# Kernel tuning notes

Measured on AMD Instinct MI355X. Metric: run time of the kernel, lower is better.

## Reference

```python
import jax, jax.numpy as jnp
import numpy as np

K = 3
STRIDE = 1
PAD = 1


def setup_inputs() -> dict:
    key = jax.random.key(0)
    k1, k2, k3 = jax.random.split(key, 3)
    N, C, H, W = 4, 256, 64, 64
    outC = 256
    x = jax.random.normal(k1, (N, C, H, W), dtype=jnp.float32)
    # offset/mask conv params (torch inits these to 0; small random makes the test nontrivial)
    conv_offset_w = jax.random.normal(k2, (3 * K * K, C, K, K), dtype=jnp.float32) * 0.01
    conv_offset_b = jnp.zeros((3 * K * K,), dtype=jnp.float32)
    # xavier-normal scale for dcn weight
    fan = C * K * K + outC * K * K
    dcn_weight = jax.random.normal(k3, (outC, C, K, K), dtype=jnp.float32) * np.float32(np.sqrt(2.0 / fan))
    return {"x": x, "conv_offset_w": conv_offset_w, "conv_offset_b": conv_offset_b, "dcn_weight": dcn_weight}


def _dcn(x, w_off, b_off, dcn_weight):
    k, s, p = K, STRIDE, PAD
    N, C, H, W = x.shape
    outC = dcn_weight.shape[0]
    KK = k * k
    # offset/mask prediction conv
    om = jax.lax.conv_general_dilated(
        x, w_off, (s, s), [(p, p), (p, p)],
        dimension_numbers=("NCHW", "OIHW", "NCHW")) + b_off[None, :, None, None]
    offset = om[:, : 2 * KK]
    mask = jax.nn.sigmoid(om[:, 2 * KK:])
    oH = (H + 2 * p - (k - 1)) // s
    oW = (W + 2 * p - (k - 1)) // s
    # pad with an extra row/col at bottom-right so floor+1 indexing is in-bounds (as in torch code)
    px = jnp.pad(x, ((0, 0), (0, 0), (p, p + 1), (p, p + 1)))
    px = jnp.transpose(px, (0, 2, 3, 1))  # (N, H+2p+1, W+2p+1, C)
    offset = jnp.transpose(offset, (0, 2, 3, 1)).reshape(N, oH, oW, KK, 2)  # (...,(y,x))
    mask = jnp.transpose(mask, (0, 2, 3, 1))  # (N, oH, oW, KK)
    base_y = jnp.arange(oH, dtype=jnp.float32) * s + p
    base_x = jnp.arange(oW, dtype=jnp.float32) * s + p
    half = (k - 1) // 2
    inner_y = jnp.repeat(jnp.arange(k, dtype=jnp.float32) - half, k)  # kernel-tap y offsets
    inner_x = jnp.tile(jnp.arange(k, dtype=jnp.float32) - half, k)   # kernel-tap x offsets
    pos_y = base_y[None, :, None, None] + inner_y[None, None, None, :] + offset[..., 0]
    pos_x = base_x[None, None, :, None] + inner_x[None, None, None, :] + offset[..., 1]
    pos_y = jnp.clip(pos_y, 0.0, H + 2 * p - 1.0)
    pos_x = jnp.clip(pos_x, 0.0, W + 2 * p - 1.0)
    y1 = jnp.floor(pos_y)
    x1 = jnp.floor(pos_x)
    y1i = y1.astype(jnp.int32)
    x1i = x1.astype(jnp.int32)
    nidx = jnp.arange(N)[:, None, None, None]
    # bilinear gathers: each (N, oH, oW, KK, C)
    v1 = px[nidx, y1i, x1i]
    v2 = px[nidx, y1i, x1i + 1]
    v3 = px[nidx, y1i + 1, x1i]
    v4 = px[nidx, y1i + 1, x1i + 1]
    lh = (pos_y - y1)[..., None]
    lw = (pos_x - x1)[..., None]
    hh = 1.0 - lh
    hw = 1.0 - lw
    value = hh * hw * v1 + hh * lw * v2 + lh * hw * v3 + lh * lw * v4
    value = value * mask[..., None]  # modulated
    w = dcn_weight.reshape(outC, C, KK)
    # sum over in_C and kernel taps -> NCHW output
    out = jnp.einsum("nhwkc,ock->nohw", value, w)
    return out


def reference(x, conv_offset_w, conv_offset_b, dcn_weight):
    return _dcn(x, conv_offset_w, conv_offset_b, dcn_weight)
```

## Files before the change

kernel.cpp:

```cpp
#include <hip/hip_runtime.h>
#include <type_traits>


typedef __bf16 bf16x8 __attribute__((ext_vector_type(8)));
typedef float  f32x4  __attribute__((ext_vector_type(4)));
typedef unsigned short ushort8 __attribute__((ext_vector_type(8)));
typedef unsigned int   uint4v  __attribute__((ext_vector_type(4)));

#define XBF_OFF   0u
#define WREP_OFF  8388608u
#define WMAIN_OFF 8536064u
#define OM_OFF    9715712u

#define LGKM0_BAR() do { __builtin_amdgcn_s_waitcnt(0xC07F); __builtin_amdgcn_s_barrier(); } while (0)

template <int N> using ic = std::integral_constant<int, N>;

__device__ __forceinline__ unsigned short f2bf(float f) {
  unsigned int u = __float_as_uint(f);
  u += 0x7fffu + ((u >> 16) & 1u);
  return (unsigned short)(u >> 16);
}
__device__ __forceinline__ float bf2f(unsigned short h) {
  return __uint_as_float(((unsigned int)h) << 16);
}

__global__ __launch_bounds__(256) void k_pre(const float* __restrict__ x,
                                             const float* __restrict__ w_off,
                                             const float* __restrict__ dcn_w,
                                             unsigned short* __restrict__ xbf,
                                             unsigned short* __restrict__ wrep,
                                             unsigned short* __restrict__ wmain) {
  __shared__ float tile[32][65];
  __shared__ unsigned short lsh[2304];
  int b = blockIdx.x;
  int t = threadIdx.x;
  if (b < 2048) {
    int n  = b >> 9;
    int cb = (b >> 6) & 7;
    int xb = b & 63;
    int xx  = t & 63;
    int cc0 = t >> 6;
#pragma unroll
    for (int j = 0; j < 8; ++j) {
      int cc = cc0 + j * 4;
      tile[cc][xx] = x[((size_t)(n * 256 + cb * 32 + cc) << 12) + xb * 64 + xx];
    }
    __syncthreads();
    int ccw = t & 31;
    int xw0 = t >> 5;
#pragma unroll
    for (int j = 0; j < 8; ++j) {
      int xw = xw0 + j * 8;
      xbf[((size_t)((n << 12) + xb * 64 + xw)) * 256 + cb * 32 + ccw] = f2bf(tile[ccw][xw]);
    }
  } else {
    int ocb = b - 2048;
    const float* src;
    unsigned short* dst;
    int oc;
    if (ocb < 32) { oc = ocb; src = w_off; dst = wrep; }
    else          { oc = ocb - 32; src = dcn_w; dst = wmain; }
    if (ocb < 32 && oc >= 27) {
#pragma unroll
      for (int j = 0; j < 9; ++j) dst[oc * 2304 + j * 256 + t] = 0;
      return;
    }
    const float* base = src + (size_t)oc * 2304;
#pragma unroll
    for (int j = 0; j < 9; ++j) lsh[j * 256 + t] = f2bf(base[t * 9 + j]);
    __syncthreads();
#pragma unroll
    for (int j = 0; j < 9; ++j) dst[oc * 2304 + j * 256 + t] = lsh[j * 256 + t];
  }
}

__global__ __launch_bounds__(1024) void k_offconv(const unsigned short* __restrict__ xbf,
                                                  const unsigned short* __restrict__ wrep,
                                                  const float* __restrict__ bias,
                                                  float* __restrict__ om) {
  __shared__ __align__(16) unsigned short SHa[4][64 * 64];
  __shared__ __align__(16) unsigned short SHb[4][32 * 64];
  int t = threadIdx.x;
  int wave = t >> 6, lane = t & 63;
  int grp = wave >> 2, wv = wave & 3;
  int tg = t & 255;
  int bm = ((blockIdx.x & 7) << 5) + (blockIdx.x >> 3);
  int n = bm >> 6, oy = bm & 63;

  unsigned short* As = SHa[grp];
  unsigned short* Bs = SHb[grp];

  int arow = tg >> 2, acc4 = tg & 3;
  int brow = tg >> 3, bch = tg & 7;

  f32x4 acc0 = {0.f, 0.f, 0.f, 0.f};
  f32x4 acc1 = {0.f, 0.f, 0.f, 0.f};

  ushort8 av[2][2]; ushort8 bv[2];
  auto prefetch = [&](int ktg, auto slotc) {
    constexpr int slot = decltype(slotc)::value;
    int kk = ktg >> 2;
    int c0 = (ktg & 3) * 64;
    int dy = kk / 3 - 1, dx = kk % 3 - 1;
    int yy = oy + dy, xxg = arow + dx;
    bool ok = ((unsigned)yy < 64u) && ((unsigned)xxg < 64u);
    const unsigned short* p = xbf + (size_t)(((n * 64 + yy) * 64 + xxg) * 256 + c0 + acc4 * 16);
#pragma unroll
    for (int g = 0; g < 2; ++g)
      av[slot][g] = ok ? *(const ushort8*)(p + g * 8) : (ushort8){0,0,0,0,0,0,0,0};
    bv[slot] = *(const ushort8*)(wrep + (size_t)brow * 2304 + ktg * 64 + bch * 8);
  };

  int k0 = grp * 9;
  prefetch(k0, ic<0>{});
  prefetch(k0 + 1, ic<1>{});
  int mr = lane & 15, q = lane >> 4;

  auto step = [&](int kt, auto slotc) {
    constexpr int slot = decltype(slotc)::value;
    LGKM0_BAR();
#pragma unroll
    for (int g = 0; g < 2; ++g) {
      int ch = (acc4 * 2 + g) ^ (arow & 7);
      *(ushort8*)&As[arow * 64 + ch * 8] = av[slot][g];
    }
    { int ch = bch ^ (brow & 7);
      *(ushort8*)&Bs[brow * 64 + ch * 8] = bv[slot]; }
    if (kt + 2 < 9) prefetch(k0 + kt + 2, slotc);
    LGKM0_BAR();
#pragma unroll
    for (int kh = 0; kh < 2; ++kh) {
      int coff = ((q + kh * 4) ^ (mr & 7)) * 8;
      bf16x8 a  = *(const bf16x8*)&As[(wv * 16 + mr) * 64 + coff];
      bf16x8 b0 = *(const bf16x8*)&Bs[mr * 64 + coff];
      bf16x8 b1 = *(const bf16x8*)&Bs[(16 + mr) * 64 + coff];
      acc0 = __builtin_amdgcn_mfma_f32_16x16x32_bf16(a, b0, acc0, 0, 0, 0);
      acc1 = __builtin_amdgcn_mfma_f32_16x16x32_bf16(a, b1, acc1, 0, 0, 0);
    }
  };
  for (int kp = 0; kp < 4; ++kp) {
    step(2 * kp, ic<0>{});
    step(2 * kp + 1, ic<1>{});
  }
  step(8, ic<0>{});

  float* scratch = (float*)&SHa[0][0];
  __syncthreads();
  if (grp > 0) {
#pragma unroll
    for (int nt = 0; nt < 2; ++nt) {
      f32x4 a = nt ? acc1 : acc0;
#pragma unroll
      for (int rg = 0; rg < 4; ++rg)
        scratch[(grp - 1) * 2048 + (wv * 16 + q * 4 + rg) * 32 + nt * 16 + mr] = a[rg];
    }
  }
  __syncthreads();
  if (grp == 0) {
    int r0 = bm * 64;
#pragma unroll
    for (int nt = 0; nt < 2; ++nt) {
      f32x4 a = nt ? acc1 : acc0;
      int oc = nt * 16 + mr;
      float bvl = (oc < 27) ? bias[oc] : 0.f;
#pragma unroll
      for (int rg = 0; rg < 4; ++rg) {
        int pl = wv * 16 + q * 4 + rg;
        float v = a[rg] + bvl + scratch[pl * 32 + oc] +
                  scratch[2048 + pl * 32 + oc] + scratch[4096 + pl * 32 + oc];
        if (oc >= 18 && oc < 27) v = 1.f / (1.f + __expf(-v));
        om[(r0 + pl) * 32 + oc] = v;
      }
    }
  }
}

__global__ __launch_bounds__(1024) void k_gemm_fused(const unsigned short* __restrict__ xbf,
                                                     const float* __restrict__ om,
                                                     const unsigned short* __restrict__ wB,
                                                     float* __restrict__ out) {
  __shared__ __align__(16) unsigned short Ab[3][128 * 64];
  __shared__ __align__(16) unsigned short Bb[3][128 * 64];
  int t = threadIdx.x;
  int wave = t >> 6, lane = t & 63;
  int wm = wave & 3, wn = wave >> 2;
  int bmx = ((blockIdx.x & 7) << 4) + (blockIdx.x >> 3);
  int r0 = bmx * 128, o0 = blockIdx.y * 128;

  int srow = t >> 3;
  int sch  = (t & 7) * 8;
  int r = r0 + srow;
  int n = r >> 12, yx = r & 4095, oy = yx >> 6, ox = yx & 63;
  const unsigned short* xb = xbf + (size_t)n * (4096 * 256);
  const float* omr = om + (size_t)r * 32;
  const unsigned short* Bg = wB + (size_t)(o0 + srow) * 2304 + sch;
  int wch = ((t & 7) ^ (srow & 7)) * 8;

  f32x4 acc[2][2];
#pragma unroll
  for (int mt = 0; mt < 2; ++mt)
#pragma unroll
    for (int nt = 0; nt < 2; ++nt) acc[mt][nt] = (f32x4){0.f, 0.f, 0.f, 0.f};

  float pv_y, pv_x, pv_m;
  float cw1, cw2, cw3, cw4;
  int a1, a2, a3, a4;
  float wbuf[2][4];

  auto loadom = [&](int kk) {
    pv_y = omr[2 * kk]; pv_x = omr[2 * kk + 1]; pv_m = omr[18 + kk];
  };
  auto params = [&](int kk) {
    float py = (float)(oy + kk / 3) + pv_y;
    float px = (float)(ox + kk % 3) + pv_x;
    float m = pv_m;
    py = fminf(fmaxf(py, 0.f), 65.f);
    px = fminf(fmaxf(px, 0.f), 65.f);
    float fy = floorf(py), fx = floorf(px);
    float ly = py - fy, lx = px - fx;
    float hy = 1.f - ly, hx = 1.f - lx;
    int iy = (int)fy, ix = (int)fx;
    bool yv0 = (iy >= 1) && (iy <= 64);
    bool yv1 = (iy <= 63);
    bool xv0 = (ix >= 1) && (ix <= 64);
    bool xv1 = (ix <= 63);
    int y0 = min(max(iy - 1, 0), 63);
    int y1 = min(iy, 63);
    int x0 = min(max(ix - 1, 0), 63);
    int x1 = min(ix, 63);
    cw1 = (yv0 && xv0) ? hy * hx * m : 0.f;
    cw2 = (yv0 && xv1) ? hy * lx * m : 0.f;
    cw3 = (yv1 && xv0) ? ly * hx * m : 0.f;
    cw4 = (yv1 && xv1) ? ly * lx * m : 0.f;
    a1 = ((y0 << 6) + x0) * 256;
    a2 = ((y0 << 6) + x1) * 256;
    a3 = ((y1 << 6) + x0) * 256;
    a4 = ((y1 << 6) + x1) * 256;
  };

  ushort8 g1[2], g2[2], g3[2], g4[2], bv[2];
  auto issueA = [&](int ktg, auto slotc) {
    constexpr int slot = decltype(slotc)::value;
    wbuf[slot][0] = cw1; wbuf[slot][1] = cw2; wbuf[slot][2] = cw3; wbuf[slot][3] = cw4;
    int c = (ktg & 3) * 64 + sch;
    g1[slot] = *(const ushort8*)(xb + a1 + c);
    g2[slot] = *(const ushort8*)(xb + a2 + c);
    g3[slot] = *(const ushort8*)(xb + a3 + c);
    g4[slot] = *(const ushort8*)(xb + a4 + c);
  };
  auto issueB = [&](int ktg, auto slotc) {
    constexpr int slot = decltype(slotc)::value;
    bv[slot] = *(const ushort8*)(Bg + ktg * 64);
  };

  loadom(0);
  params(0);
  loadom(1);
  issueA(0, ic<0>{}); issueB(0, ic<0>{});
  issueA(1, ic<1>{}); issueB(1, ic<1>{});

  int mr = lane & 15, q = lane >> 4;

  auto step = [&](int k, auto slotc, auto bufc) {
    constexpr int slot = decltype(slotc)::value;
    constexpr int buf  = decltype(bufc)::value;
    uint4v rs;
#pragma unroll
    for (int p = 0; p < 4; ++p) {
      float va = wbuf[slot][0] * bf2f(g1[slot][2 * p])     + wbuf[slot][1] * bf2f(g2[slot][2 * p]) +
                 wbuf[slot][2] * bf2f(g3[slot][2 * p])     + wbuf[slot][3] * bf2f(g4[slot][2 * p]);
      float vb = wbuf[slot][0] * bf2f(g1[slot][2 * p + 1]) + wbuf[slot][1] * bf2f(g2[slot][2 * p + 1]) +
                 wbuf[slot][2] * bf2f(g3[slot][2 * p + 1]) + wbuf[slot][3] * bf2f(g4[slot][2 * p + 1]);
      unsigned ua = __float_as_uint(va) + 0x8000u;
      unsigned ub = __float_as_uint(vb) + 0x8000u;
      rs[p] = __builtin_amdgcn_perm(ub, ua, 0x07060302u);
    }
    *(uint4v*)&Ab[buf][srow * 64 + wch] = rs;
    *(ushort8*)&Bb[buf][srow * 64 + wch] = bv[slot];
    if (k + 2 < 36) {
      if (((k + 2) & 3) == 0) {
        int kk = (k + 2) >> 2;
        params(kk);
        loadom(kk < 8 ? kk + 1 : 8);
      }
      issueA(k + 2, slotc);
      issueB(k + 2, slotc);
    }
    LGKM0_BAR();
#pragma unroll
    for (int kh = 0; kh < 2; ++kh) {
      int coff = ((q + kh * 4) ^ (mr & 7)) * 8;
      bf16x8 af[2], bfv[2];
#pragma unroll
      for (int mt = 0; mt < 2; ++mt)
        af[mt] = *(const bf16x8*)&Ab[buf][(wm * 32 + mt * 16 + mr) * 64 + coff];
#pragma unroll
      for (int nt = 0; nt < 2; ++nt)
        bfv[nt] = *(const bf16x8*)&Bb[buf][(wn * 32 + nt * 16 + mr) * 64 + coff];
#pragma unroll
      for (int mt = 0; mt < 2; ++mt)
#pragma unroll
        for (int nt = 0; nt < 2; ++nt)
          acc[mt][nt] = __builtin_amdgcn_mfma_f32_16x16x32_bf16(af[mt], bfv[nt], acc[mt][nt], 0, 0, 0);
    }
  };

  for (int kp = 0; kp < 6; ++kp) {
    int k = kp * 6;
    step(k + 0, ic<0>{}, ic<0>{});
    step(k + 1, ic<1>{}, ic<1>{});
    step(k + 2, ic<0>{}, ic<2>{});
    step(k + 3, ic<1>{}, ic<0>{});
    step(k + 4, ic<0>{}, ic<1>{});
    step(k + 5, ic<1>{}, ic<2>{});
  }

#pragma unroll
  for (int mt = 0; mt < 2; ++mt)
#pragma unroll
    for (int nt = 0; nt < 2; ++nt) {
      int p = r0 + wm * 32 + mt * 16 + q * 4;
      int o = o0 + wn * 32 + nt * 16 + mr;
      int nn = p >> 12, pyx = p & 4095;
      *(f32x4*)(out + ((size_t)(nn * 256 + o) << 12) + pyx) = acc[mt][nt];
    }
}

extern "C" void kernel_launch(void* const* d_in, const int* in_sizes, int n_in,
                              void* d_out, int out_size, void* d_ws, size_t ws_size,
                              hipStream_t stream) {
  const float* x     = (const float*)d_in[0];
  const float* w_off = (const float*)d_in[1];
  const float* b_off = (const float*)d_in[2];
  const float* dcn_w = (const float*)d_in[3];
  float* out = (float*)d_out;
  char* ws = (char*)d_ws;
  unsigned short* xbf   = (unsigned short*)(ws + XBF_OFF);
  unsigned short* wrep  = (unsigned short*)(ws + WREP_OFF);
  unsigned short* wmain = (unsigned short*)(ws + WMAIN_OFF);
  float*          om    = (float*)(ws + OM_OFF);

  k_pre<<<2048 + 288, 256, 0, stream>>>(x, w_off, dcn_w, xbf, wrep, wmain);
  k_offconv<<<256, 1024, 0, stream>>>(xbf, wrep, b_off, om);
  k_gemm_fused<<<dim3(128, 2), 1024, 0, stream>>>(xbf, om, wmain, out);
}
```

Baseline: 126.4 us.

## Compute all output channels per block with B fragments loaded directly from pre-swizzled global weights

```diff
diff --git a/kernel.cpp b/kernel.cpp
--- a/kernel.cpp
+++ b/kernel.cpp
@@ -5,7 +5,8 @@
 typedef __bf16 bf16x8 __attribute__((ext_vector_type(8)));
 typedef float  f32x4  __attribute__((ext_vector_type(4)));
 typedef unsigned short ushort8 __attribute__((ext_vector_type(8)));
-typedef unsigned int   uint4v  __attribute__((ext_vector_type(4)));
+typedef unsigned short ushort4v __attribute__((ext_vector_type(4)));
+typedef unsigned int   uint2v  __attribute__((ext_vector_type(2)));
 
 #define XBF_OFF   0u
 #define WREP_OFF  8388608u
@@ -56,22 +57,30 @@
     }
   } else {
     int ocb = b - 2048;
-    const float* src;
-    unsigned short* dst;
-    int oc;
-    if (ocb < 32) { oc = ocb; src = w_off; dst = wrep; }
-    else          { oc = ocb - 32; src = dcn_w; dst = wmain; }
-    if (ocb < 32 && oc >= 27) {
-#pragma unroll
-      for (int j = 0; j < 9; ++j) dst[oc * 2304 + j * 256 + t] = 0;
-      return;
-    }
-    const float* base = src + (size_t)oc * 2304;
-#pragma unroll
-    for (int j = 0; j < 9; ++j) lsh[j * 256 + t] = f2bf(base[t * 9 + j]);
-    __syncthreads();
-#pragma unroll
-    for (int j = 0; j < 9; ++j) dst[oc * 2304 + j * 256 + t] = lsh[j * 256 + t];
+    if (ocb < 32) {
+      int oc = ocb;
+      if (oc >= 27) {
+#pragma unroll
+        for (int j = 0; j < 9; ++j) wrep[oc * 2304 + j * 256 + t] = 0;
+        return;
+      }
+      const float* base = w_off + (size_t)oc * 2304;
+#pragma unroll
+      for (int j = 0; j < 9; ++j) lsh[j * 256 + t] = f2bf(base[t * 9 + j]);
+      __syncthreads();
+#pragma unroll
+      for (int j = 0; j < 9; ++j) wrep[oc * 2304 + j * 256 + t] = lsh[j * 256 + t];
+    } else {
+      int oc = ocb - 32;
+      const float* base = dcn_w + (size_t)oc * 2304;
+      int oco = ((oc >> 4) << 9) + (oc & 15) * 8;
+#pragma unroll
+      for (int j = 0; j < 9; ++j) {
+        int k = j * 256 + t;
+        wmain[((k >> 5) << 13) + oco + (((k >> 3) & 3) << 7) + (k & 7)] =
+            f2bf(base[t * 9 + j]);
+      }
+    }
   }
 }
 
@@ -180,22 +189,23 @@
                                                      const float* __restrict__ om,
                                                      const unsigned short* __restrict__ wB,
                                                      float* __restrict__ out) {
-  __shared__ __align__(16) unsigned short Ab[3][128 * 64];
-  __shared__ __align__(16) unsigned short Bb[3][128 * 64];
+  __shared__ __align__(16) unsigned short Ab[3][64 * 64];
   int t = threadIdx.x;
   int wave = t >> 6, lane = t & 63;
-  int wm = wave & 3, wn = wave >> 2;
-  int bmx = ((blockIdx.x & 7) << 4) + (blockIdx.x >> 3);
-  int r0 = bmx * 128, o0 = blockIdx.y * 128;
-
-  int srow = t >> 3;
-  int sch  = (t & 7) * 8;
+  int wm = wave & 1, wn = wave >> 1;
+  int bmx = ((blockIdx.x & 7) << 5) + (blockIdx.x >> 3);
+  int r0 = bmx * 64;
+
+  int srow = t >> 4;
+  int sch  = (t & 15) * 4;
   int r = r0 + srow;
   int n = r >> 12, yx = r & 4095, oy = yx >> 6, ox = yx & 63;
   const unsigned short* xb = xbf + (size_t)n * (4096 * 256);
   const float* omr = om + (size_t)r * 32;
-  const unsigned short* Bg = wB + (size_t)(o0 + srow) * 2304 + sch;
-  int wch = ((t & 7) ^ (srow & 7)) * 8;
+  int wch = ((((t >> 1) & 7) ^ (srow & 7)) << 3) + (t & 1) * 4;
+
+  int mr = lane & 15, q = lane >> 4;
+  const unsigned short* Bb0 = wB + wn * 1024 + lane * 8;
 
   f32x4 acc[2][2];
 #pragma unroll
@@ -239,35 +249,41 @@
     a4 = ((y1 << 6) + x1) * 256;
   };
 
-  ushort8 g1[2], g2[2], g3[2], g4[2], bv[2];
+  ushort4v g1[2], g2[2], g3[2], g4[2];
+  bf16x8 bfr[2][4];
+
   auto issueA = [&](int ktg, auto slotc) {
     constexpr int slot = decltype(slotc)::value;
     wbuf[slot][0] = cw1; wbuf[slot][1] = cw2; wbuf[slot][2] = cw3; wbuf[slot][3] = cw4;
     int c = (ktg & 3) * 64 + sch;
-    g1[slot] = *(const ushort8*)(xb + a1 + c);
-    g2[slot] = *(const ushort8*)(xb + a2 + c);
-    g3[slot] = *(const ushort8*)(xb + a3 + c);
-    g4[slot] = *(const ushort8*)(xb + a4 + c);
+    g1[slot] = *(const ushort4v*)(xb + a1 + c);
+    g2[slot] = *(const ushort4v*)(xb + a2 + c);
+    g3[slot] = *(const ushort4v*)(xb + a3 + c);
+    g4[slot] = *(const ushort4v*)(xb + a4 + c);
   };
   auto issueB = [&](int ktg, auto slotc) {
     constexpr int slot = decltype(slotc)::value;
-    bv[slot] = *(const ushort8*)(Bg + ktg * 64);
+#pragma unroll
+    for (int kh = 0; kh < 2; ++kh)
+#pragma unroll
+      for (int nt = 0; nt < 2; ++nt)
+        bfr[slot][kh * 2 + nt] =
+            *(const bf16x8*)(Bb0 + (size_t)(ktg * 2 + kh) * 8192 + nt * 512);
   };
 
   loadom(0);
   params(0);
   loadom(1);
-  issueA(0, ic<0>{}); issueB(0, ic<0>{});
-  issueA(1, ic<1>{}); issueB(1, ic<1>{});
-
-  int mr = lane & 15, q = lane >> 4;
+  issueA(0, ic<0>{});
+  issueA(1, ic<1>{});
+  issueB(0, ic<0>{});
 
   auto step = [&](int k, auto slotc, auto bufc) {
     constexpr int slot = decltype(slotc)::value;
     constexpr int buf  = decltype(bufc)::value;
-    uint4v rs;
-#pragma unroll
-    for (int p = 0; p < 4; ++p) {
+    uint2v rs;
+#pragma unroll
+    for (int p = 0; p < 2; ++p) {
       float va = wbuf[slot][0] * bf2f(g1[slot][2 * p])     + wbuf[slot][1] * bf2f(g2[slot][2 * p]) +
                  wbuf[slot][2] * bf2f(g3[slot][2 * p])     + wbuf[slot][3] * bf2f(g4[slot][2 * p]);
       float vb = wbuf[slot][0] * bf2f(g1[slot][2 * p + 1]) + wbuf[slot][1] * bf2f(g2[slot][2 * p + 1]) +
@@ -276,8 +292,7 @@
       unsigned ub = __float_as_uint(vb) + 0x8000u;
       rs[p] = __builtin_amdgcn_perm(ub, ua, 0x07060302u);
     }
-    *(uint4v*)&Ab[buf][srow * 64 + wch] = rs;
-    *(ushort8*)&Bb[buf][srow * 64 + wch] = bv[slot];
+    *(uint2v*)&Ab[buf][srow * 64 + wch] = rs;
     if (k + 2 < 36) {
       if (((k + 2) & 3) == 0) {
         int kk = (k + 2) >> 2;
@@ -285,24 +300,18 @@
         loadom(kk < 8 ? kk + 1 : 8);
       }
       issueA(k + 2, slotc);
-      issueB(k + 2, slotc);
-    }
+    }
+    if (k + 1 < 36) issueB(k + 1, ic<1 - slot>{});
     LGKM0_BAR();
 #pragma unroll
     for (int kh = 0; kh < 2; ++kh) {
       int coff = ((q + kh * 4) ^ (mr & 7)) * 8;
-      bf16x8 af[2], bfv[2];
-#pragma unroll
-      for (int mt = 0; mt < 2; ++mt)
-        af[mt] = *(const bf16x8*)&Ab[buf][(wm * 32 + mt * 16 + mr) * 64 + coff];
-#pragma unroll
-      for (int nt = 0; nt < 2; ++nt)
-        bfv[nt] = *(const bf16x8*)&Bb[buf][(wn * 32 + nt * 16 + mr) * 64 + coff];
-#pragma unroll
-      for (int mt = 0; mt < 2; ++mt)
-#pragma unroll
-        for (int nt = 0; nt < 2; ++nt)
-          acc[mt][nt] = __builtin_amdgcn_mfma_f32_16x16x32_bf16(af[mt], bfv[nt], acc[mt][nt], 0, 0, 0);
+      bf16x8 af0 = *(const bf16x8*)&Ab[buf][(wm * 32 + mr) * 64 + coff];
+      bf16x8 af1 = *(const bf16x8*)&Ab[buf][(wm * 32 + 16 + mr) * 64 + coff];
+      acc[0][0] = __builtin_amdgcn_mfma_f32_16x16x32_bf16(af0, bfr[slot][kh * 2 + 0], acc[0][0], 0, 0, 0);
+      acc[0][1] = __builtin_amdgcn_mfma_f32_16x16x32_bf16(af0, bfr[slot][kh * 2 + 1], acc[0][1], 0, 0, 0);
+      acc[1][0] = __builtin_amdgcn_mfma_f32_16x16x32_bf16(af1, bfr[slot][kh * 2 + 0], acc[1][0], 0, 0, 0);
+      acc[1][1] = __builtin_amdgcn_mfma_f32_16x16x32_bf16(af1, bfr[slot][kh * 2 + 1], acc[1][1], 0, 0, 0);
     }
   };
 
@@ -321,7 +330,7 @@
 #pragma unroll
     for (int nt = 0; nt < 2; ++nt) {
       int p = r0 + wm * 32 + mt * 16 + q * 4;
-      int o = o0 + wn * 32 + nt * 16 + mr;
+      int o = wn * 32 + nt * 16 + mr;
       int nn = p >> 12, pyx = p & 4095;
       *(f32x4*)(out + ((size_t)(nn * 256 + o) << 12) + pyx) = acc[mt][nt];
     }
@@ -343,5 +352,5 @@
 
   k_pre<<<2048 + 288, 256, 0, stream>>>(x, w_off, dcn_w, xbf, wrep, wmain);
   k_offconv<<<256, 1024, 0, stream>>>(xbf, wrep, b_off, om);
-  k_gemm_fused<<<dim3(128, 2), 1024, 0, stream>>>(xbf, om, wmain, out);
-}
+  k_gemm_fused<<<256, 1024, 0, stream>>>(xbf, om, wmain, out);
+}
```

Measured after the change: 132.3 us. 4.7% more time.

## Warp-specialize fused DCN GEMM into producer gather waves and MFMA consumer waves

Applied to the files above, without the earlier changes.

```diff
diff --git a/kernel.cpp b/kernel.cpp
--- a/kernel.cpp
+++ b/kernel.cpp
@@ -176,155 +176,170 @@
   }
 }
 
-__global__ __launch_bounds__(1024) void k_gemm_fused(const unsigned short* __restrict__ xbf,
-                                                     const float* __restrict__ om,
-                                                     const unsigned short* __restrict__ wB,
-                                                     float* __restrict__ out) {
-  __shared__ __align__(16) unsigned short Ab[3][128 * 64];
-  __shared__ __align__(16) unsigned short Bb[3][128 * 64];
+__global__ __launch_bounds__(768, 3) void k_gemm_fused(const unsigned short* __restrict__ xbf,
+                                                       const float* __restrict__ om,
+                                                       const unsigned short* __restrict__ wB,
+                                                       float* __restrict__ out) {
+  __shared__ __align__(16) unsigned short Ab[2][64 * 64];
+  __shared__ __align__(16) unsigned short Bb[2][256 * 64];
   int t = threadIdx.x;
   int wave = t >> 6, lane = t & 63;
-  int wm = wave & 3, wn = wave >> 2;
-  int bmx = ((blockIdx.x & 7) << 4) + (blockIdx.x >> 3);
-  int r0 = bmx * 128, o0 = blockIdx.y * 128;
-
-  int srow = t >> 3;
-  int sch  = (t & 7) * 8;
-  int r = r0 + srow;
-  int n = r >> 12, yx = r & 4095, oy = yx >> 6, ox = yx & 63;
-  const unsigned short* xb = xbf + (size_t)n * (4096 * 256);
-  const float* omr = om + (size_t)r * 32;
-  const unsigned short* Bg = wB + (size_t)(o0 + srow) * 2304 + sch;
-  int wch = ((t & 7) ^ (srow & 7)) * 8;
-
-  f32x4 acc[2][2];
-#pragma unroll
-  for (int mt = 0; mt < 2; ++mt)
-#pragma unroll
-    for (int nt = 0; nt < 2; ++nt) acc[mt][nt] = (f32x4){0.f, 0.f, 0.f, 0.f};
-
-  float pv_y, pv_x, pv_m;
-  float cw1, cw2, cw3, cw4;
-  int a1, a2, a3, a4;
-  float wbuf[2][4];
-
-  auto loadom = [&](int kk) {
-    pv_y = omr[2 * kk]; pv_x = omr[2 * kk + 1]; pv_m = omr[18 + kk];
-  };
-  auto params = [&](int kk) {
-    float py = (float)(oy + kk / 3) + pv_y;
-    float px = (float)(ox + kk % 3) + pv_x;
-    float m = pv_m;
-    py = fminf(fmaxf(py, 0.f), 65.f);
-    px = fminf(fmaxf(px, 0.f), 65.f);
-    float fy = floorf(py), fx = floorf(px);
-    float ly = py - fy, lx = px - fx;
-    float hy = 1.f - ly, hx = 1.f - lx;
-    int iy = (int)fy, ix = (int)fx;
-    bool yv0 = (iy >= 1) && (iy <= 64);
-    bool yv1 = (iy <= 63);
-    bool xv0 = (ix >= 1) && (ix <= 64);
-    bool xv1 = (ix <= 63);
-    int y0 = min(max(iy - 1, 0), 63);
-    int y1 = min(iy, 63);
-    int x0 = min(max(ix - 1, 0), 63);
-    int x1 = min(ix, 63);
-    cw1 = (yv0 && xv0) ? hy * hx * m : 0.f;
-    cw2 = (yv0 && xv1) ? hy * lx * m : 0.f;
-    cw3 = (yv1 && xv0) ? ly * hx * m : 0.f;
-    cw4 = (yv1 && xv1) ? ly * lx * m : 0.f;
-    a1 = ((y0 << 6) + x0) * 256;
-    a2 = ((y0 << 6) + x1) * 256;
-    a3 = ((y1 << 6) + x0) * 256;
-    a4 = ((y1 << 6) + x1) * 256;
-  };
-
-  ushort8 g1[2], g2[2], g3[2], g4[2], bv[2];
-  auto issueA = [&](int ktg, auto slotc) {
-    constexpr int slot = decltype(slotc)::value;
-    wbuf[slot][0] = cw1; wbuf[slot][1] = cw2; wbuf[slot][2] = cw3; wbuf[slot][3] = cw4;
-    int c = (ktg & 3) * 64 + sch;
-    g1[slot] = *(const ushort8*)(xb + a1 + c);
-    g2[slot] = *(const ushort8*)(xb + a2 + c);
-    g3[slot] = *(const ushort8*)(xb + a3 + c);
-    g4[slot] = *(const ushort8*)(xb + a4 + c);
-  };
-  auto issueB = [&](int ktg, auto slotc) {
-    constexpr int slot = decltype(slotc)::value;
-    bv[slot] = *(const ushort8*)(Bg + ktg * 64);
-  };
-
-  loadom(0);
-  params(0);
-  loadom(1);
-  issueA(0, ic<0>{}); issueB(0, ic<0>{});
-  issueA(1, ic<1>{}); issueB(1, ic<1>{});
-
-  int mr = lane & 15, q = lane >> 4;
-
-  auto step = [&](int k, auto slotc, auto bufc) {
-    constexpr int slot = decltype(slotc)::value;
-    constexpr int buf  = decltype(bufc)::value;
-    uint4v rs;
-#pragma unroll
-    for (int p = 0; p < 4; ++p) {
-      float va = wbuf[slot][0] * bf2f(g1[slot][2 * p])     + wbuf[slot][1] * bf2f(g2[slot][2 * p]) +
-                 wbuf[slot][2] * bf2f(g3[slot][2 * p])     + wbuf[slot][3] * bf2f(g4[slot][2 * p]);
-      float vb = wbuf[slot][0] * bf2f(g1[slot][2 * p + 1]) + wbuf[slot][1] * bf2f(g2[slot][2 * p + 1]) +
-                 wbuf[slot][2] * bf2f(g3[slot][2 * p + 1]) + wbuf[slot][3] * bf2f(g4[slot][2 * p + 1]);
-      unsigned ua = __float_as_uint(va) + 0x8000u;
-      unsigned ub = __float_as_uint(vb) + 0x8000u;
-      rs[p] = __builtin_amdgcn_perm(ub, ua, 0x07060302u);
-    }
-    *(uint4v*)&Ab[buf][srow * 64 + wch] = rs;
-    *(ushort8*)&Bb[buf][srow * 64 + wch] = bv[slot];
-    if (k + 2 < 36) {
-      if (((k + 2) & 3) == 0) {
-        int kk = (k + 2) >> 2;
-        params(kk);
-        loadom(kk < 8 ? kk + 1 : 8);
-      }
-      issueA(k + 2, slotc);
-      issueB(k + 2, slotc);
+  int bmx = ((blockIdx.x & 7) << 5) + (blockIdx.x >> 3);
+  int r0 = bmx * 64;
+
+  if (wave < 4) {
+    int wn = wave;
+    int mr = lane & 15, q = lane >> 4;
+    f32x4 acc[4][4];
+#pragma unroll
+    for (int mt = 0; mt < 4; ++mt)
+#pragma unroll
+      for (int nt = 0; nt < 4; ++nt) acc[mt][nt] = (f32x4){0.f, 0.f, 0.f, 0.f};
+
+    for (int p = 0; p < 37; ++p) {
+      if (p >= 1) {
+        int buf = (p - 1) & 1;
+#pragma unroll
+        for (int kh = 0; kh < 2; ++kh) {
+          int coff = ((q + kh * 4) ^ (mr & 7)) * 8;
+          bf16x8 af[4], bfv[4];
+#pragma unroll
+          for (int mt = 0; mt < 4; ++mt)
+            af[mt] = *(const bf16x8*)&Ab[buf][(mt * 16 + mr) * 64 + coff];
+#pragma unroll
+          for (int nt = 0; nt < 4; ++nt)
+            bfv[nt] = *(const bf16x8*)&Bb[buf][(wn * 64 + nt * 16 + mr) * 64 + coff];
+#pragma unroll
+          for (int mt = 0; mt < 4; ++mt)
+#pragma unroll
+            for (int nt = 0; nt < 4; ++nt)
+              acc[mt][nt] = __builtin_amdgcn_mfma_f32_16x16x32_bf16(af[mt], bfv[nt], acc[mt][nt], 0, 0, 0);
+        }
+      }
+      LGKM0_BAR();
+    }
+
+#pragma unroll
+    for (int mt = 0; mt < 4; ++mt)
+#pragma unroll
+      for (int nt = 0; nt < 4; ++nt) {
+        int p = r0 + mt * 16 + q * 4;
+        int o = wn * 64 + nt * 16 + mr;
+        int nn = p >> 12, pyx = p & 4095;
+        *(f32x4*)(out + ((size_t)(nn * 256 + o) << 12) + pyx) = acc[mt][nt];
+      }
+  } else {
+    int pt = t - 256;
+    int srow = pt >> 3, sch = (pt & 7) * 8;
+    int r = r0 + srow;
+    int n = r >> 12, yx = r & 4095, oy = yx >> 6, ox = yx & 63;
+    const unsigned short* xb = xbf + (size_t)n * (4096 * 256);
+    const float* omr = om + (size_t)r * 32;
+    int wchA = (((pt & 7) ^ (srow & 7)) << 3);
+    int prow = pt >> 1;
+    int pc0 = (pt & 1) * 4;
+    const unsigned short* Bg = wB + (size_t)prow * 2304 + pc0 * 8;
+    int bsw0 = (((pc0 + 0) ^ (prow & 7)) << 3);
+    int bsw1 = (((pc0 + 1) ^ (prow & 7)) << 3);
+    int bsw2 = (((pc0 + 2) ^ (prow & 7)) << 3);
+    int bsw3 = (((pc0 + 3) ^ (prow & 7)) << 3);
+
+    float pv_y, pv_x, pv_m;
+    float cw1, cw2, cw3, cw4;
+    int a1, a2, a3, a4;
+    float wbuf[2][4];
+    ushort8 g1[2], g2[2], g3[2], g4[2];
+    uint4v bvp[2][4];
+
+    auto loadom = [&](int kk) {
+      pv_y = omr[2 * kk]; pv_x = omr[2 * kk + 1]; pv_m = omr[18 + kk];
+    };
+    auto params = [&](int kk) {
+      float py = (float)(oy + kk / 3) + pv_y;
+      float px = (float)(ox + kk % 3) + pv_x;
+      float m = pv_m;
+      py = fminf(fmaxf(py, 0.f), 65.f);
+      px = fminf(fmaxf(px, 0.f), 65.f);
+      float fy = floorf(py), fx = floorf(px);
+      float ly = py - fy, lx = px - fx;
+      float hy = 1.f - ly, hx = 1.f - lx;
+      int iy = (int)fy, ix = (int)fx;
+      bool yv0 = (iy >= 1) && (iy <= 64);
+      bool yv1 = (iy <= 63);
+      bool xv0 = (ix >= 1) && (ix <= 64);
+      bool xv1 = (ix <= 63);
+      int y0 = min(max(iy - 1, 0), 63);
+      int y1 = min(iy, 63);
+      int x0 = min(max(ix - 1, 0), 63);
+      int x1 = min(ix, 63);
+      cw1 = (yv0 && xv0) ? hy * hx * m : 0.f;
+      cw2 = (yv0 && xv1) ? hy * lx * m : 0.f;
+      cw3 = (yv1 && xv0) ? ly * hx * m : 0.f;
+      cw4 = (yv1 && xv1) ? ly * lx * m : 0.f;
+      a1 = ((y0 << 6) + x0) * 256;
+      a2 = ((y0 << 6) + x1) * 256;
+      a3 = ((y1 << 6) + x0) * 256;
+      a4 = ((y1 << 6) + x1) * 256;
+    };
+
+    auto issueA = [&](int ktg, auto slotc) {
+      constexpr int slot = decltype(slotc)::value;
+      wbuf[slot][0] = cw1; wbuf[slot][1] = cw2; wbuf[slot][2] = cw3; wbuf[slot][3] = cw4;
+      int c = (ktg & 3) * 64 + sch;
+      g1[slot] = *(const ushort8*)(xb + a1 + c);
+      g2[slot] = *(const ushort8*)(xb + a2 + c);
+      g3[slot] = *(const ushort8*)(xb + a3 + c);
+      g4[slot] = *(const ushort8*)(xb + a4 + c);
+    };
+    auto issueB = [&](int ktg, auto slotc) {
+      constexpr int slot = decltype(slotc)::value;
+#pragma unroll
+      for (int j = 0; j < 4; ++j)
+        bvp[slot][j] = *(const uint4v*)(Bg + (size_t)ktg * 64 + j * 8);
+    };
+
+    loadom(0);
+    params(0);
+    loadom(1);
+    issueA(0, ic<0>{});
+    issueB(0, ic<0>{});
+
+    auto pphase = [&](int p, auto slotc) {
+      constexpr int slot = decltype(slotc)::value;
+      if (p + 1 < 36) {
+        if (((p + 1) & 3) == 0) {
+          int kk = (p + 1) >> 2;
+          params(kk);
+          loadom(kk < 8 ? kk + 1 : 8);
+        }
+        issueA(p + 1, ic<1 - slot>{});
+        issueB(p + 1, ic<1 - slot>{});
+      }
+      uint4v rs;
+#pragma unroll
+      for (int pp = 0; pp < 4; ++pp) {
+        float va = wbuf[slot][0] * bf2f(g1[slot][2 * pp])     + wbuf[slot][1] * bf2f(g2[slot][2 * pp]) +
+                   wbuf[slot][2] * bf2f(g3[slot][2 * pp])     + wbuf[slot][3] * bf2f(g4[slot][2 * pp]);
+        float vb = wbuf[slot][0] * bf2f(g1[slot][2 * pp + 1]) + wbuf[slot][1] * bf2f(g2[slot][2 * pp + 1]) +
+                   wbuf[slot][2] * bf2f(g3[slot][2 * pp + 1]) + wbuf[slot][3] * bf2f(g4[slot][2 * pp + 1]);
+        unsigned ua = __float_as_uint(va) + 0x8000u;
+        unsigned ub = __float_as_uint(vb) + 0x8000u;
+        rs[pp] = __builtin_amdgcn_perm(ub, ua, 0x07060302u);
+      }
+      *(uint4v*)&Ab[slot][srow * 64 + wchA] = rs;
+      *(uint4v*)&Bb[slot][prow * 64 + bsw0] = bvp[slot][0];
+      *(uint4v*)&Bb[slot][prow * 64 + bsw1] = bvp[slot][1];
+      *(uint4v*)&Bb[slot][prow * 64 + bsw2] = bvp[slot][2];
+      *(uint4v*)&Bb[slot][prow * 64 + bsw3] = bvp[slot][3];
+      LGKM0_BAR();
+    };
+
+    for (int pp = 0; pp < 18; ++pp) {
+      pphase(2 * pp, ic<0>{});
+      pphase(2 * pp + 1, ic<1>{});
     }
     LGKM0_BAR();
-#pragma unroll
-    for (int kh = 0; kh < 2; ++kh) {
-      int coff = ((q + kh * 4) ^ (mr & 7)) * 8;
-      bf16x8 af[2], bfv[2];
-#pragma unroll
-      for (int mt = 0; mt < 2; ++mt)
-        af[mt] = *(const bf16x8*)&Ab[buf][(wm * 32 + mt * 16 + mr) * 64 + coff];
-#pragma unroll
-      for (int nt = 0; nt < 2; ++nt)
-        bfv[nt] = *(const bf16x8*)&Bb[buf][(wn * 32 + nt * 16 + mr) * 64 + coff];
-#pragma unroll
-      for (int mt = 0; mt < 2; ++mt)
-#pragma unroll
-        for (int nt = 0; nt < 2; ++nt)
-          acc[mt][nt] = __builtin_amdgcn_mfma_f32_16x16x32_bf16(af[mt], bfv[nt], acc[mt][nt], 0, 0, 0);
-    }
-  };
-
-  for (int kp = 0; kp < 6; ++kp) {
-    int k = kp * 6;
-    step(k + 0, ic<0>{}, ic<0>{});
-    step(k + 1, ic<1>{}, ic<1>{});
-    step(k + 2, ic<0>{}, ic<2>{});
-    step(k + 3, ic<1>{}, ic<0>{});
-    step(k + 4, ic<0>{}, ic<1>{});
-    step(k + 5, ic<1>{}, ic<2>{});
-  }
-
-#pragma unroll
-  for (int mt = 0; mt < 2; ++mt)
-#pragma unroll
-    for (int nt = 0; nt < 2; ++nt) {
-      int p = r0 + wm * 32 + mt * 16 + q * 4;
-      int o = o0 + wn * 32 + nt * 16 + mr;
-      int nn = p >> 12, pyx = p & 4095;
-      *(f32x4*)(out + ((size_t)(nn * 256 + o) << 12) + pyx) = acc[mt][nt];
-    }
+  }
 }
 
 extern "C" void kernel_launch(void* const* d_in, const int* in_sizes, int n_in,
@@ -343,5 +358,5 @@
 
   k_pre<<<2048 + 288, 256, 0, stream>>>(x, w_off, dcn_w, xbf, wrep, wmain);
   k_offconv<<<256, 1024, 0, stream>>>(xbf, wrep, b_off, om);
-  k_gemm_fused<<<dim3(128, 2), 1024, 0, stream>>>(xbf, om, wmain, out);
-}
+  k_gemm_fused<<<256, 768, 0, stream>>>(xbf, om, wmain, out);
+}
```

Measured after the change: 126.8 us. Within noise of the previous version (+0.3%).
